# Performance work log

Measured on AMD Instinct MI355X. Metric: run time of the kernel, lower is better.

The kernel has to match this reference:

```python
import jax, jax.numpy as jnp
import numpy as np

B, N, D, Y = 4, 2048, 512, 8921


def setup_inputs() -> dict:
    key = jax.random.key(0)
    ks = jax.random.split(key, 9)
    scale = 1.0 / np.sqrt(D)
    return {
        "x": jax.random.normal(ks[0], (B, N, D), jnp.float32),
        "target": (jax.random.uniform(ks[1], (B, Y), jnp.float32) > 0.98).astype(jnp.float32),
        "y_flow": jax.random.normal(ks[2], (B, Y), jnp.float32),
        "U_w": jax.random.normal(ks[3], (Y, D), jnp.float32) * scale,
        "Ug_w": jax.random.normal(ks[4], (Y, D), jnp.float32) * scale,
        "final_w": jax.random.normal(ks[5], (Y, D), jnp.float32) * scale,
        "final_b": jax.random.normal(ks[6], (Y,), jnp.float32) * scale,
        "gate_w": jax.random.normal(ks[7], (D,), jnp.float32) * scale,
        "gate_b": jax.random.normal(ks[8], (), jnp.float32) * scale,
    }


def reference(x, target, y_flow, U_w, Ug_w, final_w, final_b, gate_w, gate_b):
    # Label attention branch: alpha = softmax(U_w @ x^T) over tokens -> [B, Y, N]
    alpha = jax.nn.softmax(jnp.einsum("yd,bnd->byn", U_w, x), axis=-1)
    m = jnp.einsum("byn,bnd->byd", alpha, x)  # [B, Y, D]

    # Gate attention branch
    alpha_g = jax.nn.softmax(jnp.einsum("yd,bnd->byn", Ug_w, x), axis=-1)
    m_g = jnp.einsum("byn,bnd->byd", alpha_g, x)  # [B, Y, D]

    # gate = tanh(Linear(D,1)(m_gate)) -> [B, Y]
    gate = jnp.tanh(jnp.einsum("byd,d->by", m_g, gate_w) + gate_b)

    # y = sum_d(final_w * m) + final_b + y_flow * gate
    y = jnp.einsum("yd,byd->by", final_w, m) + final_b + y_flow * gate

    # BCEWithLogitsLoss (mean): logaddexp(0, y) - y * target, numerically stable
    loss = jnp.mean(jnp.logaddexp(0.0, y) - y * target)
    return (y, loss)
```

## Files before the change

### kernel.cpp

```cpp
#include <hip/hip_runtime.h>
#include <stdint.h>

#define BQ 4
#define NQ 2048
#define DQ 512
#define YQ 8921
#define YGRP 140
#define NH 4
#define NCHQ 32
#define NUNITS (YGRP * BQ * NH)
#define NLP 140
#define GXOFF 65536
#define L2E 1.44269504088896340736f

typedef __attribute__((ext_vector_type(8))) short bf16x8;
typedef __attribute__((ext_vector_type(4))) float f32x4;

__device__ inline short f2bf(float f) {
  unsigned u = __float_as_uint(f);
  u += 0x7fffu + ((u >> 16) & 1u);
  return (short)(u >> 16);
}

__device__ inline bf16x8 pack8(float4 a, float4 b) {
  bf16x8 h;
  h[0] = f2bf(a.x); h[1] = f2bf(a.y); h[2] = f2bf(a.z); h[3] = f2bf(a.w);
  h[4] = f2bf(b.x); h[5] = f2bf(b.y); h[6] = f2bf(b.z); h[7] = f2bf(b.w);
  return h;
}

__device__ inline void gl_lds16(const void* g, void* l) {
  __builtin_amdgcn_global_load_lds((const __attribute__((address_space(1))) void*)g,
                                   (__attribute__((address_space(3))) void*)l, 16, 0, 0);
}

__global__ __launch_bounds__(256) void prep_gx(const float* __restrict__ x,
                                               const float* __restrict__ gate_w,
                                               float* __restrict__ gx) {
  int rid = blockIdx.x * 4 + (threadIdx.x >> 6);
  int lane = threadIdx.x & 63;
  const float* src = x + (size_t)rid * DQ + lane * 8;
  float4 v0 = *(const float4*)src;
  float4 v1 = *(const float4*)(src + 4);
  const float* gwp = gate_w + lane * 8;
  float s = v0.x * gwp[0] + v0.y * gwp[1] + v0.z * gwp[2] + v0.w * gwp[3]
          + v1.x * gwp[4] + v1.y * gwp[5] + v1.z * gwp[6] + v1.w * gwp[7];
#pragma unroll
  for (int d = 1; d < 64; d <<= 1) s += __shfl_xor(s, d);
  if (lane == 0) gx[rid] = s;
}

__global__ __launch_bounds__(256) void prep_xfrag(const float* __restrict__ x,
                                                  char* __restrict__ ws_x2) {
  __shared__ float xs[16 * 512];
  int t = blockIdx.x;
  const float* src = x + ((size_t)t << 13);
  int tid = threadIdx.x;
#pragma unroll
  for (int i = 0; i < 8; ++i)
    *(float4*)(xs + i * 1024 + tid * 4) = *(const float4*)(src + i * 1024 + tid * 4);
  __syncthreads();
  char* dst = ws_x2 + ((size_t)t << 14);
#pragma unroll
  for (int i = 0; i < 4; ++i) {
    int s = i * 256 + tid;
    int l = s & 63, kk = s >> 6;
    int row = l & 15, g = l >> 4;
    const float* p = xs + row * 512 + kk * 32 + g * 8;
    *(bf16x8*)(dst + s * 16) = pack8(*(const float4*)p, *(const float4*)(p + 4));
  }
}

__global__ __launch_bounds__(256) void prep_w(const float* __restrict__ Uw,
                                              const float* __restrict__ Gw,
                                              const float* __restrict__ Fw,
                                              char* __restrict__ ws_w) {
  int rid = blockIdx.x * 4 + (threadIdx.x >> 6);
  if (rid >= 3 * YQ) return;
  int lane = threadIdx.x & 63;
  int mat = rid / YQ, y = rid % YQ;
  const float* src = (mat == 0 ? Uw : (mat == 1 ? Gw : Fw)) + (size_t)y * DQ + lane * 8;
  *(bf16x8*)(ws_w + (size_t)rid * 1024 + lane * 16) =
      pack8(*(const float4*)src, *(const float4*)(src + 4));
}

template<bool FULL>
__global__ __launch_bounds__(256, 2) void fused_kernel(
    const float* __restrict__ x, const char* __restrict__ ws_x2,
    const char* __restrict__ ws_w,
    const float* __restrict__ Uw, const float* __restrict__ Gw,
    const float* __restrict__ Fw, const float* __restrict__ gx,
    float4* __restrict__ ws_state) {
  extern __shared__ char smem[];
  const int tid = threadIdx.x, l = tid & 63, w = tid >> 6;
  const int lr = l & 15, lg4 = l >> 4;
  int u = (blockIdx.x & 7) * (NUNITS / 8) + (blockIdx.x >> 3);
  const int b = u / (YGRP * NH);
  const int r0 = u % (YGRP * NH);
  const int yg = r0 / NH, nh = r0 % NH;
  const int ybase = yg * 64 + w * 16;
  const int nbase = nh * (NQ / NH);

  bf16x8 wU[16], wG[16], wF[16];
  {
    int y = ybase + lr; if (y >= YQ) y = YQ - 1;
    if constexpr (FULL) {
      const char* p0 = ws_w + ((size_t)y * DQ + lg4 * 8) * 2;
#pragma unroll
      for (int kk = 0; kk < 16; ++kk) {
        wU[kk] = *(const bf16x8*)(p0 + kk * 64);
        wG[kk] = *(const bf16x8*)(p0 + (size_t)YQ * 1024 + kk * 64);
        wF[kk] = *(const bf16x8*)(p0 + (size_t)YQ * 2048 + kk * 64);
      }
    } else {
      const float* pu = Uw + (size_t)y * DQ + lg4 * 8;
      const float* pg = Gw + (size_t)y * DQ + lg4 * 8;
      const float* pf = Fw + (size_t)y * DQ + lg4 * 8;
#pragma unroll
      for (int kk = 0; kk < 16; ++kk) {
        wU[kk] = pack8(*(const float4*)(pu + kk * 32), *(const float4*)(pu + kk * 32 + 4));
        wG[kk] = pack8(*(const float4*)(pg + kk * 32), *(const float4*)(pg + kk * 32 + 4));
        wF[kk] = pack8(*(const float4*)(pf + kk * 32), *(const float4*)(pf + kk * 32 + 4));
      }
    }
  }

  float lU = 0.f, aU = 0.f, lG = 0.f, aG = 0.f;

  if constexpr (FULL) {
    {
      float2 g2 = *(const float2*)(gx + b * NQ + nbase + tid * 2);
      *(float2*)(smem + GXOFF + tid * 8) = g2;
    }
    const char* xb = ws_x2 + (((size_t)(b * 128 + nh * 32)) << 14);
    auto stage = [&](int c) {
      const char* src = xb + ((size_t)c << 14);
      char* lb = smem + (c & 3) * 16384;
#pragma unroll
      for (int j = 0; j < 4; ++j) {
        int s = w * 4 + j;
        gl_lds16(src + s * 1024 + l * 16, lb + s * 1024);
      }
    };
    stage(0); stage(1); stage(2);
    asm volatile("s_waitcnt vmcnt(8)" ::: "memory");
    __syncthreads();

#pragma unroll 1
    for (int c = 0; c < NCHQ; ++c) {
      if (c + 3 < NCHQ) stage(c + 3);
      const char* ab = smem + (c & 3) * 16384 + l * 16;
      f32x4 sU = {0.f, 0.f, 0.f, 0.f}, sG = sU, sF = sU;
#pragma unroll
      for (int kk = 0; kk < 16; ++kk) {
        bf16x8 a = *(const bf16x8*)(ab + kk * 1024);
        sU = __builtin_amdgcn_mfma_f32_16x16x32_bf16(a, wU[kk], sU, 0, 0, 0);
        sG = __builtin_amdgcn_mfma_f32_16x16x32_bf16(a, wG[kk], sG, 0, 0, 0);
        sF = __builtin_amdgcn_mfma_f32_16x16x32_bf16(a, wF[kk], sF, 0, 0, 0);
      }
      float4 gxv = *(const float4*)(smem + GXOFF + c * 64 + lg4 * 16);
      float gv[4] = {gxv.x, gxv.y, gxv.z, gxv.w};
#pragma unroll
      for (int r = 0; r < 4; ++r) {
        float eu = __builtin_amdgcn_exp2f(sU[r] * L2E);
        lU += eu; aU = fmaf(eu, sF[r], aU);
        float eg = __builtin_amdgcn_exp2f(sG[r] * L2E);
        lG += eg; aG = fmaf(eg, gv[r], aG);
      }
      int rem = NCHQ - 1 - c;
      if (rem >= 3)      asm volatile("s_waitcnt vmcnt(8)" ::: "memory");
      else if (rem == 2) asm volatile("s_waitcnt vmcnt(4)" ::: "memory");
      else if (rem == 1) asm volatile("s_waitcnt vmcnt(0)" ::: "memory");
      if (rem >= 1) {
        __builtin_amdgcn_sched_barrier(0);
        __builtin_amdgcn_s_barrier();
      }
    }
  } else {
    const float* gxb = gx + b * NQ + nbase + lg4 * 4;
    for (int c = 0; c < NCHQ; ++c) {
      __syncthreads();
#pragma unroll
      for (int j = 0; j < 4; ++j) {
        int slot = j * 256 + tid;
        int kk = slot >> 6, l2 = slot & 63;
        int row = l2 & 15, g4 = l2 >> 4;
        const float* g = x + ((size_t)(b * NQ + nbase + c * 16 + row)) * DQ
                       + kk * 32 + g4 * 8;
        *(bf16x8*)(smem + slot * 16) = pack8(*(const float4*)g, *(const float4*)(g + 4));
      }
      __syncthreads();
      const char* ab = smem + l * 16;
      f32x4 sU = {0.f, 0.f, 0.f, 0.f}, sG = sU, sF = sU;
#pragma unroll
      for (int kk = 0; kk < 16; ++kk) {
        bf16x8 a = *(const bf16x8*)(ab + kk * 1024);
        sU = __builtin_amdgcn_mfma_f32_16x16x32_bf16(a, wU[kk], sU, 0, 0, 0);
        sG = __builtin_amdgcn_mfma_f32_16x16x32_bf16(a, wG[kk], sG, 0, 0, 0);
        sF = __builtin_amdgcn_mfma_f32_16x16x32_bf16(a, wF[kk], sF, 0, 0, 0);
      }
      float4 gxv = *(const float4*)(gxb + c * 16);
      float gv[4] = {gxv.x, gxv.y, gxv.z, gxv.w};
#pragma unroll
      for (int r = 0; r < 4; ++r) {
        float eu = __builtin_amdgcn_exp2f(sU[r] * L2E);
        lU += eu; aU = fmaf(eu, sF[r], aU);
        float eg = __builtin_amdgcn_exp2f(sG[r] * L2E);
        lG += eg; aG = fmaf(eg, gv[r], aG);
      }
    }
  }

#pragma unroll
  for (int d = 16; d < 64; d <<= 1) {
    lU += __shfl_xor(lU, d); aU += __shfl_xor(aU, d);
    lG += __shfl_xor(lG, d); aG += __shfl_xor(aG, d);
  }

  int y = ybase + lr;
  if (lg4 == 0 && y < YQ) {
    float4 st; st.x = lU; st.y = aU; st.z = lG; st.w = aG;
    ws_state[(size_t)(b * NH + nh) * YQ + y] = st;
  }
}

__global__ __launch_bounds__(256) void merge_kernel(
    const float4* __restrict__ ws_state, const float* __restrict__ fb,
    const float* __restrict__ gate_b, const float* __restrict__ yflow,
    const float* __restrict__ target, float* __restrict__ out_y,
    float* __restrict__ loss_part) {
  __shared__ float sb[256];
  int t = blockIdx.x * 256 + threadIdx.x;
  float lt = 0.f;
  if (t < BQ * YQ) {
    int b = t / YQ, y = t % YQ;
    float lU = 0.f, aU = 0.f, lG = 0.f, aG = 0.f;
#pragma unroll
    for (int nh = 0; nh < NH; ++nh) {
      float4 s = ws_state[(size_t)(b * NH + nh) * YQ + y];
      lU += s.x; aU += s.y; lG += s.z; aG += s.w;
    }
    float gate = tanhf(aG / lG + gate_b[0]);
    float yv = aU / lU + fb[y] + yflow[t] * gate;
    out_y[t] = yv;
    float tg = target[t];
    lt = fmaxf(yv, 0.f) + log1pf(__expf(-fabsf(yv))) - yv * tg;
  }
  sb[threadIdx.x] = lt;
  __syncthreads();
  for (int st = 128; st > 0; st >>= 1) {
    if (threadIdx.x < st) sb[threadIdx.x] += sb[threadIdx.x + st];
    __syncthreads();
  }
  if (threadIdx.x == 0) loss_part[blockIdx.x] = sb[0];
}

__global__ __launch_bounds__(256) void loss_kernel(const float* __restrict__ lp,
                                                   float* __restrict__ out) {
  __shared__ float sb[256];
  float s = (threadIdx.x < NLP) ? lp[threadIdx.x] : 0.f;
  sb[threadIdx.x] = s;
  __syncthreads();
  for (int st = 128; st > 0; st >>= 1) {
    if (threadIdx.x < st) sb[threadIdx.x] += sb[threadIdx.x + st];
    __syncthreads();
  }
  if (threadIdx.x == 0) out[BQ * YQ] = sb[0] / (float)(BQ * YQ);
}

extern "C" void kernel_launch(void* const* d_in, const int* in_sizes, int n_in,
                              void* d_out, int out_size, void* d_ws, size_t ws_size,
                              hipStream_t stream) {
  const float* x      = (const float*)d_in[0];
  const float* target = (const float*)d_in[1];
  const float* yflow  = (const float*)d_in[2];
  const float* Uw     = (const float*)d_in[3];
  const float* Gw     = (const float*)d_in[4];
  const float* Fw     = (const float*)d_in[5];
  const float* fb     = (const float*)d_in[6];
  const float* gw     = (const float*)d_in[7];
  const float* gb     = (const float*)d_in[8];
  float* out = (float*)d_out;
  char* ws = (char*)d_ws;

  const size_t xbytes  = (size_t)BQ * NQ * DQ * 2;
  const size_t wbytes  = (size_t)3 * YQ * DQ * 2;
  const size_t gxbytes = (size_t)BQ * NQ * 4;
  const size_t stbytes = (size_t)BQ * NH * YQ * 16;
  const size_t lpbytes = (size_t)NLP * 4;
  const bool full = ws_size >= xbytes + wbytes + gxbytes + stbytes + lpbytes;

  char* ws_x2; char* ws_w; float* gxp; float4* stp; float* lp;
  if (full) {
    ws_x2 = ws; ws_w = ws + xbytes;
    gxp = (float*)(ws + xbytes + wbytes);
    stp = (float4*)(ws + xbytes + wbytes + gxbytes);
    lp  = (float*)(ws + xbytes + wbytes + gxbytes + stbytes);
  } else {
    ws_x2 = nullptr; ws_w = nullptr;
    gxp = (float*)ws;
    stp = (float4*)(ws + gxbytes);
    lp  = (float*)(ws + gxbytes + stbytes);
  }

  (void)hipFuncSetAttribute(reinterpret_cast<const void*>(&fused_kernel<true>),
                            hipFuncAttributeMaxDynamicSharedMemorySize, 67584);
  (void)hipFuncSetAttribute(reinterpret_cast<const void*>(&fused_kernel<false>),
                            hipFuncAttributeMaxDynamicSharedMemorySize, 16384);

  prep_gx<<<dim3(2048), 256, 0, stream>>>(x, gw, gxp);
  if (full) {
    prep_xfrag<<<dim3(BQ * 128), 256, 0, stream>>>(x, ws_x2);
    prep_w<<<dim3((3 * YQ + 3) / 4), 256, 0, stream>>>(Uw, Gw, Fw, ws_w);
    fused_kernel<true ><<<dim3(NUNITS), 256, 67584, stream>>>(
        x, ws_x2, ws_w, Uw, Gw, Fw, gxp, stp);
  } else {
    fused_kernel<false><<<dim3(NUNITS), 256, 16384, stream>>>(
        x, ws_x2, ws_w, Uw, Gw, Fw, gxp, stp);
  }
  merge_kernel<<<dim3(NLP), 256, 0, stream>>>(stp, fb, gb, yflow, target, out, lp);
  loss_kernel<<<1, 256, 0, stream>>>(lp, out);
}
```

Baseline: 224.0 us.

## Load x fragments directly into registers with ping-pong software pipelining

Replaces the LDS staging pipeline (async global-to-LDS loads with a 4-deep ring buffer and per-chunk barriers) with direct global loads of x fragments into two register buffers. It alternates even and odd tiles so that the softmax exp/accumulate of one tile overlaps the MFMAs of the next. LDS shrinks to the gx vector only, and launch bounds drop to 1 block per SIMD-group to make room for the larger register footprint. The risks are lower occupancy, register spills, and redundant global/L2 reads, because each of the four waves now loads the same x tile itself.

```diff
diff --git a/kernel.cpp b/kernel.cpp
--- a/kernel.cpp
+++ b/kernel.cpp
@@ -7,10 +7,9 @@
 #define YQ 8921
 #define YGRP 140
 #define NH 4
-#define NCHQ 32
+#define NTIL 32
 #define NUNITS (YGRP * BQ * NH)
 #define NLP 140
-#define GXOFF 65536
 #define L2E 1.44269504088896340736f
 
 typedef __attribute__((ext_vector_type(8))) short bf16x8;
@@ -27,11 +26,6 @@
   h[0] = f2bf(a.x); h[1] = f2bf(a.y); h[2] = f2bf(a.z); h[3] = f2bf(a.w);
   h[4] = f2bf(b.x); h[5] = f2bf(b.y); h[6] = f2bf(b.z); h[7] = f2bf(b.w);
   return h;
-}
-
-__device__ inline void gl_lds16(const void* g, void* l) {
-  __builtin_amdgcn_global_load_lds((const __attribute__((address_space(1))) void*)g,
-                                   (__attribute__((address_space(3))) void*)l, 16, 0, 0);
 }
 
 __global__ __launch_bounds__(256) void prep_gx(const float* __restrict__ x,
@@ -85,7 +79,7 @@
 }
 
 template<bool FULL>
-__global__ __launch_bounds__(256, 2) void fused_kernel(
+__global__ __launch_bounds__(256, 1) void fused_kernel(
     const float* __restrict__ x, const char* __restrict__ ws_x2,
     const char* __restrict__ ws_w,
     const float* __restrict__ Uw, const float* __restrict__ Gw,
@@ -128,65 +122,100 @@
   float lU = 0.f, aU = 0.f, lG = 0.f, aG = 0.f;
 
   if constexpr (FULL) {
+    *(float2*)(smem + tid * 8) = *(const float2*)(gx + b * NQ + nbase + tid * 2);
+    __syncthreads();
+
+    const char* xb = ws_x2 + (((size_t)(b * 128 + nh * 32)) << 14) + l * 16;
+    bf16x8 bA[16], bB[16];
+#pragma unroll
+    for (int kk = 0; kk < 16; ++kk) bA[kk] = *(const bf16x8*)(xb + kk * 1024);
+
+    f32x4 eU, eG, eF;
+    f32x4 oU, oG, oF;
+#pragma unroll
+    for (int r = 0; r < 4; ++r) { oU[r] = -1e30f; oG[r] = -1e30f; oF[r] = 0.f; }
+
+#pragma unroll 1
+    for (int si = 0; si < 4; ++si) {
+#pragma unroll
+      for (int pi = 0; pi < 4; ++pi) {
+        const int p = si * 4 + pi;
+        const int tE = 2 * p, tO = 2 * p + 1;
+        {
+          const char* src = xb + ((size_t)tO << 14);
+#pragma unroll
+          for (int kk = 0; kk < 16; ++kk) bB[kk] = *(const bf16x8*)(src + kk * 1024);
+        }
+#pragma unroll
+        for (int r = 0; r < 4; ++r) { eU[r] = 0.f; eG[r] = 0.f; eF[r] = 0.f; }
+#pragma unroll
+        for (int kk = 0; kk < 16; ++kk) {
+          eU = __builtin_amdgcn_mfma_f32_16x16x32_bf16(bA[kk], wU[kk], eU, 0, 0, 0);
+          eG = __builtin_amdgcn_mfma_f32_16x16x32_bf16(bA[kk], wG[kk], eG, 0, 0, 0);
+          eF = __builtin_amdgcn_mfma_f32_16x16x32_bf16(bA[kk], wF[kk], eF, 0, 0, 0);
+        }
+        {
+          const int tp = (tE > 0) ? (tE - 1) : 0;
+          float4 gv = *(const float4*)(smem + tp * 64 + lg4 * 16);
+          float g4[4] = {gv.x, gv.y, gv.z, gv.w};
+#pragma unroll
+          for (int r = 0; r < 4; ++r) {
+            float eu = __builtin_amdgcn_exp2f(oU[r] * L2E);
+            lU += eu; aU = fmaf(eu, oF[r], aU);
+            float eg = __builtin_amdgcn_exp2f(oG[r] * L2E);
+            lG += eg; aG = fmaf(eg, g4[r], aG);
+          }
+        }
+        {
+          const int tn = (tE + 2 < NTIL) ? (tE + 2) : (NTIL - 1);
+          const char* src = xb + ((size_t)tn << 14);
+#pragma unroll
+          for (int kk = 0; kk < 16; ++kk) bA[kk] = *(const bf16x8*)(src + kk * 1024);
+        }
+#pragma unroll
+        for (int r = 0; r < 4; ++r) { oU[r] = 0.f; oG[r] = 0.f; oF[r] = 0.f; }
+#pragma unroll
+        for (int kk = 0; kk < 16; ++kk) {
+          oU = __builtin_amdgcn_mfma_f32_16x16x32_bf16(bB[kk], wU[kk], oU, 0, 0, 0);
+          oG = __builtin_amdgcn_mfma_f32_16x16x32_bf16(bB[kk], wG[kk], oG, 0, 0, 0);
+          oF = __builtin_amdgcn_mfma_f32_16x16x32_bf16(bB[kk], wF[kk], oF, 0, 0, 0);
+        }
+        {
+          float4 gv = *(const float4*)(smem + tE * 64 + lg4 * 16);
+          float g4[4] = {gv.x, gv.y, gv.z, gv.w};
+#pragma unroll
+          for (int r = 0; r < 4; ++r) {
+            float eu = __builtin_amdgcn_exp2f(eU[r] * L2E);
+            lU += eu; aU = fmaf(eu, eF[r], aU);
+            float eg = __builtin_amdgcn_exp2f(eG[r] * L2E);
+            lG += eg; aG = fmaf(eg, g4[r], aG);
+          }
+        }
+      }
+      __builtin_amdgcn_s_barrier();
+    }
     {
-      float2 g2 = *(const float2*)(gx + b * NQ + nbase + tid * 2);
-      *(float2*)(smem + GXOFF + tid * 8) = g2;
-    }
-    const char* xb = ws_x2 + (((size_t)(b * 128 + nh * 32)) << 14);
-    auto stage = [&](int c) {
-      const char* src = xb + ((size_t)c << 14);
-      char* lb = smem + (c & 3) * 16384;
-#pragma unroll
-      for (int j = 0; j < 4; ++j) {
-        int s = w * 4 + j;
-        gl_lds16(src + s * 1024 + l * 16, lb + s * 1024);
-      }
-    };
-    stage(0); stage(1); stage(2);
-    asm volatile("s_waitcnt vmcnt(8)" ::: "memory");
-    __syncthreads();
-
-#pragma unroll 1
-    for (int c = 0; c < NCHQ; ++c) {
-      if (c + 3 < NCHQ) stage(c + 3);
-      const char* ab = smem + (c & 3) * 16384 + l * 16;
-      f32x4 sU = {0.f, 0.f, 0.f, 0.f}, sG = sU, sF = sU;
-#pragma unroll
-      for (int kk = 0; kk < 16; ++kk) {
-        bf16x8 a = *(const bf16x8*)(ab + kk * 1024);
-        sU = __builtin_amdgcn_mfma_f32_16x16x32_bf16(a, wU[kk], sU, 0, 0, 0);
-        sG = __builtin_amdgcn_mfma_f32_16x16x32_bf16(a, wG[kk], sG, 0, 0, 0);
-        sF = __builtin_amdgcn_mfma_f32_16x16x32_bf16(a, wF[kk], sF, 0, 0, 0);
-      }
-      float4 gxv = *(const float4*)(smem + GXOFF + c * 64 + lg4 * 16);
-      float gv[4] = {gxv.x, gxv.y, gxv.z, gxv.w};
+      float4 gv = *(const float4*)(smem + (NTIL - 1) * 64 + lg4 * 16);
+      float g4[4] = {gv.x, gv.y, gv.z, gv.w};
 #pragma unroll
       for (int r = 0; r < 4; ++r) {
-        float eu = __builtin_amdgcn_exp2f(sU[r] * L2E);
-        lU += eu; aU = fmaf(eu, sF[r], aU);
-        float eg = __builtin_amdgcn_exp2f(sG[r] * L2E);
-        lG += eg; aG = fmaf(eg, gv[r], aG);
-      }
-      int rem = NCHQ - 1 - c;
-      if (rem >= 3)      asm volatile("s_waitcnt vmcnt(8)" ::: "memory");
-      else if (rem == 2) asm volatile("s_waitcnt vmcnt(4)" ::: "memory");
-      else if (rem == 1) asm volatile("s_waitcnt vmcnt(0)" ::: "memory");
-      if (rem >= 1) {
-        __builtin_amdgcn_sched_barrier(0);
-        __builtin_amdgcn_s_barrier();
+        float eu = __builtin_amdgcn_exp2f(oU[r] * L2E);
+        lU += eu; aU = fmaf(eu, oF[r], aU);
+        float eg = __builtin_amdgcn_exp2f(oG[r] * L2E);
+        lG += eg; aG = fmaf(eg, g4[r], aG);
       }
     }
   } else {
     const float* gxb = gx + b * NQ + nbase + lg4 * 4;
-    for (int c = 0; c < NCHQ; ++c) {
+    for (int c = 0; c < NTIL; ++c) {
       __syncthreads();
 #pragma unroll
       for (int j = 0; j < 4; ++j) {
         int slot = j * 256 + tid;
         int kk = slot >> 6, l2 = slot & 63;
-        int row = l2 & 15, g4 = l2 >> 4;
+        int row = l2 & 15, g4i = l2 >> 4;
         const float* g = x + ((size_t)(b * NQ + nbase + c * 16 + row)) * DQ
-                       + kk * 32 + g4 * 8;
+                       + kk * 32 + g4i * 8;
         *(bf16x8*)(smem + slot * 16) = pack8(*(const float4*)g, *(const float4*)(g + 4));
       }
       __syncthreads();
@@ -303,16 +332,11 @@
     lp  = (float*)(ws + gxbytes + stbytes);
   }
 
-  (void)hipFuncSetAttribute(reinterpret_cast<const void*>(&fused_kernel<true>),
-                            hipFuncAttributeMaxDynamicSharedMemorySize, 67584);
-  (void)hipFuncSetAttribute(reinterpret_cast<const void*>(&fused_kernel<false>),
-                            hipFuncAttributeMaxDynamicSharedMemorySize, 16384);
-
   prep_gx<<<dim3(2048), 256, 0, stream>>>(x, gw, gxp);
   if (full) {
     prep_xfrag<<<dim3(BQ * 128), 256, 0, stream>>>(x, ws_x2);
     prep_w<<<dim3((3 * YQ + 3) / 4), 256, 0, stream>>>(Uw, Gw, Fw, ws_w);
-    fused_kernel<true ><<<dim3(NUNITS), 256, 67584, stream>>>(
+    fused_kernel<true ><<<dim3(NUNITS), 256, 2048, stream>>>(
         x, ws_x2, ws_w, Uw, Gw, Fw, gxp, stp);
   } else {
     fused_kernel<false><<<dim3(NUNITS), 256, 16384, stream>>>(
```

Measured after the change: 583.8 us. 2.61x slower.
